# Kernel optimization log

Measured on AMD Instinct MI355X. Metric: run time of the kernel, lower is better.

## Reference

```python
import jax, jax.numpy as jnp
import numpy as np

B, C, D, H, W = 2, 2, 64, 256, 256
EPS = 1e-6
ALPHA = 5.0
TTEMP = 0.7


def _grids():
    gy, gx = jnp.meshgrid(jnp.arange(H, dtype=jnp.float32),
                          jnp.arange(W, dtype=jnp.float32), indexing='ij')
    return gy, gx


def _extract_targets(centerlines, gy, gx):
    # centerlines: [B,1,D,H,W] int labels {0,1,2}. For each (b,d) slice: if label i
    # occurs exactly once, target = (y,x) of that pixel, else negpair (-1,-1).
    cl = centerlines[:, 0]  # [B,D,H,W]
    out = []
    for lbl in (1, 2):
        m = (cl == lbl).astype(jnp.float32)
        cnt = m.sum(axis=(-2, -1))            # [B,D]
        ys = (m * gy).sum(axis=(-2, -1))
        xs = (m * gx).sum(axis=(-2, -1))
        t = jnp.where((cnt == 1.0)[..., None], jnp.stack([ys, xs], axis=-1), -1.0)
        out.append(t)                          # [B,D,2] float32
    return out


def _d2(gy, gx, target):
    # torch PairwiseDistance adds eps to the difference: ||x1-x2+eps||_2
    # -> [B,1,D,H,W]
    dy = gy[None, None, None] - target[:, None, :, 0, None, None] + EPS
    dx = gx[None, None, None] - target[:, None, :, 1, None, None] + EPS
    return jnp.sqrt(dy * dy + dx * dx)


def total_loss(logits, centerlines, radiuses):
    probs = jax.nn.sigmoid(logits)             # [B,2,D,H,W]
    gy, gx = _grids()
    targets = _extract_targets(centerlines, gy, gx)
    d2s = [_d2(gy, gx, t) for t in targets]
    # art masks: relu(exp(d2/r1 - 1) - 1) then filled with 1 where >0  ==  (d2 > r1);
    # the in-place fill makes it gradient-free, so treat as constant {0,1} mask.
    arts = [jax.lax.stop_gradient((d2s[k] > radiuses[k, 1]).astype(jnp.float32))
            for k in range(2)]
    arts = [arts[1], arts[0]]                  # swapped, exactly as in the source
    valid = [(t[:, :, 0] != -1.0).astype(jnp.float32) for t in targets]  # [B,D]

    # ---- CenterDistanceLoss ----
    loss_cent = jnp.float32(0.0)
    for k in range(2):
        art = arts[k]                                            # [B,1,D,H,W]
        denom = (probs * art).sum(axis=(1, 3, 4)) + EPS          # [B,D]
        y_cnt = (art * gy * probs).sum(axis=(1, 3, 4)) / denom
        x_cnt = (art * gx * probs).sum(axis=(1, 3, 4)) / denom
        cnt = jnp.stack([y_cnt, x_cnt], axis=-1)                 # [B,D,2]
        diff = cnt - targets[k] + EPS
        l2 = jnp.sqrt((diff * diff).sum(-1)) * valid[k]
        loss_cent = loss_cent + l2.mean()

    # ---- RadiusConstraintLoss ----
    loss_cnst = jnp.float32(0.0)
    for k in range(2):
        r_lu, r_ow = radiuses[k, 0], radiuses[k, 1]
        vm = valid[k][:, None, :, None, None]                    # [B,1,D,1,1]
        d2 = d2s[k]
        art = arts[k]
        lu_dout = jax.nn.relu(1.0 - jnp.exp(1.0 - d2 / r_lu)) / ALPHA * vm * art
        ow_dout = jax.nn.relu(1.0 - jnp.exp(1.0 - d2 / r_ow)) / ALPHA * vm * art
        p_lu, p_ow = probs[:, :1], probs[:, 1:]
        rc_out = ((lu_dout * p_lu).sum(axis=(1, 3, 4)) / (p_lu.sum(axis=(1, 3, 4)) + EPS)
                  + (ow_dout * p_ow).sum(axis=(1, 3, 4)) / (p_ow.sum(axis=(1, 3, 4)) + EPS))
        lu_din = jax.nn.relu(jnp.exp(1.0 - d2 / r_lu) - 1.0) * vm
        ow_din = jax.nn.relu(jnp.exp(1.0 - d2 / r_ow) - 1.0) * vm
        rc_in = ((lu_din * (1.0 - p_lu)).sum(axis=(1, 3, 4)) / (r_lu * r_lu * jnp.pi)
                 + (ow_din * (1.0 - p_ow)).sum(axis=(1, 3, 4)) / (r_ow * r_ow * jnp.pi))
        loss_cnst = loss_cnst + rc_out.mean() + rc_in.mean()

    # ---- ConsistencyLoss ----  (F.softmax default dim=1 for 5-D; BCE clamps log >= -100)
    p_orig = jax.lax.stop_gradient(jax.nn.softmax(logits[:, :, 1:-1] / TTEMP, axis=1))
    p_shift = jax.nn.softmax(logits[:, :, 0:-2] / TTEMP, axis=1)
    log_p = jnp.maximum(jnp.log(p_orig), -100.0)
    log_1mp = jnp.maximum(jnp.log(1.0 - p_orig), -100.0)
    loss_csis = -(p_shift * log_p + (1.0 - p_shift) * log_1mp).mean()

    return 0.02 * loss_cent + 1.0 * loss_cnst + 0.001 * loss_csis


def setup_inputs():
    key = jax.random.key(0)
    k1, k2, k3, k4, k5 = jax.random.split(key, 5)
    logits = jax.random.normal(k1, (B, C, D, H, W), dtype=jnp.float32)
    # place exactly one ICA(=1) and one ECA(=2) marker per (b,d) slice
    ys1 = jax.random.randint(k2, (B * D,), 0, H)
    xs1 = jax.random.randint(k3, (B * D,), 0, W)
    ys2 = jax.random.randint(k4, (B * D,), 0, H)
    xs2 = jax.random.randint(k5, (B * D,), 0, W)
    bi = jnp.repeat(jnp.arange(B), D)
    di = jnp.tile(jnp.arange(D), B)
    cl = jnp.zeros((B, 1, D, H, W), dtype=jnp.int32)
    cl = cl.at[bi, 0, di, ys1, xs1].set(1)
    cl = cl.at[bi, 0, di, ys2, xs2].set(2)
    cl = cl.at[:, :, 0].set(0)  # exercise the negpair (-1,-1) path
    radiuses = jnp.array([[4.0, 7.0], [5.0, 8.0]], dtype=jnp.float32)
    return {"logits": logits, "centerlines": cl, "radiuses": radiuses}


def reference(logits, centerlines, radiuses):
    return total_loss(logits, centerlines, radiuses)
```

## Files before the change

### kernel.cpp

```cpp
#include <hip/hip_runtime.h>
#include <math.h>

#define BB 2
#define CC 2
#define DD 64
#define HW 65536
#define NROW 128
#define EPSF 1e-6f
#define ALPHAF 5.0f
#define LOG2E 1.44269504089f
#define LN2 0.69314718056f
#define INV_T (1.0f/0.7f)
#define C_SH (INV_T*LOG2E)

struct Ws {
  float tgt[2][NROW][2];
  float valid[2][NROW];
  float part[NROW][2][17];
};

struct RowCtx {
  float t0y, t0x, t1y, t1x;
  float r01sq, r11sq;
  float c00, c01, c10, c11;
};

template<bool N0, bool N1>
__device__ __forceinline__ void do_row(const float4& v0, const float4& v1,
                                       const float4& w0, const float4& w1,
                                       float yf, float x0f,
                                       const RowCtx& cx, float* acc)
{
  const float a0[4] = {v0.x, v0.y, v0.z, v0.w};
  const float a1[4] = {v1.x, v1.y, v1.z, v1.w};
  const float b0[4] = {w0.x, w0.y, w0.z, w0.w};
  const float b1[4] = {w1.x, w1.y, w1.z, w1.w};
  float rp0 = 0.f, rp1 = 0.f, rprod = 0.f, rsp = 0.f, rpsx = 0.f;
  float rA0 = 0.f, rA0x = 0.f, rT00 = 0.f, rT01 = 0.f;
  float rA1 = 0.f, rA1x = 0.f, rT10 = 0.f, rT11 = 0.f;
  const float dy0 = yf - cx.t0y;
  const float dy0sq = dy0 * dy0;
  const float dy1 = yf - cx.t1y;
  const float dy1sq = dy1 * dy1;
#pragma unroll
  for (int e = 0; e < 4; ++e) {
    const float le0 = a0[e], le1 = a1[e];
    const float p0 = __builtin_amdgcn_rcpf(1.f + __expf(-le0));
    const float p1 = __builtin_amdgcn_rcpf(1.f + __expf(-le1));
    rp0 += p0; rp1 += p1;
    const float psum = p0 + p1;
    const float gxf = x0f + (float)e;

    const float t = (le1 - le0) * C_SH;
    const float E = exp2f(-fabsf(t));
    const float R = __builtin_amdgcn_rcpf(1.f + E);
    const float L = log2f(1.f + E);
    const float psig = (t >= 0.f ? E : 1.f) * R;
    const float dorn = (b0[e] - b1[e]) * C_SH;
    rprod = fmaf(psig, dorn, rprod);
    rsp  += fmaxf(-t, 0.f) + L;

    float ap0 = p0, ap1 = p1, bp0 = p0, bp1 = p1;
    float d0sq = 0.f, d1sq = 0.f;
    if (N1) {
      const float dx1 = gxf - cx.t1x;
      d1sq = fmaf(dx1, dx1, dy1sq);
      const float art0 = (d1sq > cx.r11sq) ? 1.f : 0.f;
      ap0 = art0 * p0; ap1 = art0 * p1;
      const float a0p = ap0 + ap1;
      rA0 += a0p; rA0x = fmaf(gxf, a0p, rA0x);
      if (!N0) { rT00 += ap0; rT01 += ap1; }
    }
    if (N0) {
      const float dx0 = gxf - cx.t0x;
      d0sq = fmaf(dx0, dx0, dy0sq);
      const float art1 = (d0sq > cx.r01sq) ? 1.f : 0.f;
      bp0 = art1 * p0; bp1 = art1 * p1;
      const float a1p = bp0 + bp1;
      rA1 += a1p; rA1x = fmaf(gxf, a1p, rA1x);
      if (!N1) { rT10 += bp0; rT11 += bp1; }
    }
    if (!N0 || !N1) rpsx = fmaf(gxf, psum, rpsx);

    if (N0) {
      const float dist0 = __builtin_amdgcn_sqrtf(d0sq);
      const float elu0 = exp2f(fmaf(dist0, -cx.c00, LOG2E));
      const float eow0 = exp2f(fmaf(dist0, -cx.c01, LOG2E));
      acc[8]  = fmaf(fmaxf(1.f - elu0, 0.f), ap0, acc[8]);
      acc[9]  = fmaf(fmaxf(1.f - eow0, 0.f), ap1, acc[9]);
      acc[10] = fmaf(fmaxf(elu0 - 1.f, 0.f), 1.f - p0, acc[10]);
      acc[11] = fmaf(fmaxf(eow0 - 1.f, 0.f), 1.f - p1, acc[11]);
    }
    if (N1) {
      const float dist1 = __builtin_amdgcn_sqrtf(d1sq);
      const float elu1 = exp2f(fmaf(dist1, -cx.c10, LOG2E));
      const float eow1 = exp2f(fmaf(dist1, -cx.c11, LOG2E));
      acc[12] = fmaf(fmaxf(1.f - elu1, 0.f), bp0, acc[12]);
      acc[13] = fmaf(fmaxf(1.f - eow1, 0.f), bp1, acc[13]);
      acc[14] = fmaf(fmaxf(elu1 - 1.f, 0.f), 1.f - p0, acc[14]);
      acc[15] = fmaf(fmaxf(eow1 - 1.f, 0.f), 1.f - p1, acc[15]);
    }
  }
  acc[6] += rp0; acc[7] += rp1; acc[16] += rprod; acc[17] += rsp;
  const float rps = rp0 + rp1;
  if (N1) { acc[0] += rA0; acc[1] = fmaf(yf, rA0, acc[1]); acc[2] += rA0x; }
  else    { acc[0] += rps; acc[1] = fmaf(yf, rps, acc[1]); acc[2] += rpsx; }
  if (N0) { acc[3] += rA1; acc[4] = fmaf(yf, rA1, acc[4]); acc[5] += rA1x; }
  else    { acc[3] += rps; acc[4] = fmaf(yf, rps, acc[4]); acc[5] += rpsx; }
  if (!N0) { acc[8]  += N1 ? rT00 : rp0; acc[9]  += N1 ? rT01 : rp1; }
  if (!N1) { acc[12] += N0 ? rT10 : rp0; acc[13] += N0 ? rT11 : rp1; }
}

#define DISPATCH_ROW(V0,V1,W0,W1,YF)                                       \
  { const bool nr0 = fabsf((YF) - cx.t0y) <= cut0;                         \
    const bool nr1 = fabsf((YF) - cx.t1y) <= cut1;                         \
    if (nr0) { if (nr1) do_row<true ,true >(V0,V1,W0,W1,YF,x0f,cx,acc);    \
               else     do_row<true ,false>(V0,V1,W0,W1,YF,x0f,cx,acc); }  \
    else     { if (nr1) do_row<false,true >(V0,V1,W0,W1,YF,x0f,cx,acc);    \
               else     do_row<false,false>(V0,V1,W0,W1,YF,x0f,cx,acc); } }

__global__ __launch_bounds__(1024) void k_all(const float* __restrict__ logits,
                                              const int* __restrict__ cl,
                                              const float* __restrict__ rad,
                                              Ws* __restrict__ ws)
{
  const int xcd  = blockIdx.x & 7;
  const int slot = blockIdx.x >> 3;
  const int row  = xcd * 16 + (slot >> 1);
  const int half = slot & 1;
  const int tid  = threadIdx.x;
  const int lane = tid & 63;
  const int wid  = tid >> 6;
  const int b = row >> 6, d = row & 63;

  const float* l0 = logits + (((long long)(b * CC + 0) * DD + d) << 16);
  const float* l1 = logits + (((long long)(b * CC + 1) * DD + d) << 16);
  const bool csa = (d < DD - 2);
  const bool csb = (d >= 1) && (d <= DD - 2);
  const long long noff = csa ? HW : 0;
  const float* m0 = l0 + noff;
  const float* m1 = l1 + noff;

  const float x0f = (float)(lane << 2);
  int y = half + (wid << 1);
  int p = (y << 8) + (lane << 2);

  float4 v0 = *(const float4*)(l0 + p);
  float4 v1 = *(const float4*)(l1 + p);
  float4 w0 = *(const float4*)(m0 + p);
  float4 w1 = *(const float4*)(m1 + p);

  __shared__ int sacc[6];
  if (tid < 6) sacc[tid] = 0;
  __syncthreads();
  {
    const int4* cp = (const int4*)(cl + ((long long)row << 16));
#pragma unroll 8
    for (int j = 0; j < 16; ++j) {
      const int idx4 = tid + (j << 10);
      const int4 v = cp[idx4];
      if ((v.x | v.y | v.z | v.w) != 0) {
        const int vv[4] = {v.x, v.y, v.z, v.w};
#pragma unroll
        for (int e = 0; e < 4; ++e) {
          const int val = vv[e];
          if (val == 1 || val == 2) {
            const int hw = (idx4 << 2) + e;
            const int k3 = (val - 1) * 3;
            atomicAdd(&sacc[k3 + 0], 1);
            atomicAdd(&sacc[k3 + 1], hw >> 8);
            atomicAdd(&sacc[k3 + 2], hw & 255);
          }
        }
      }
    }
  }
  __syncthreads();
  const int c0 = sacc[0], c1 = sacc[3];
  const float t0y = (c0 == 1) ? (float)sacc[1] : -1.f;
  const float t0x = (c0 == 1) ? (float)sacc[2] : -1.f;
  const float t1y = (c1 == 1) ? (float)sacc[4] : -1.f;
  const float t1x = (c1 == 1) ? (float)sacc[5] : -1.f;
  if (half == 0 && tid == 0) {
    ws->tgt[0][row][0] = t0y; ws->tgt[0][row][1] = t0x;
    ws->valid[0][row] = (c0 == 1) ? 1.f : 0.f;
    ws->tgt[1][row][0] = t1y; ws->tgt[1][row][1] = t1x;
    ws->valid[1][row] = (c1 == 1) ? 1.f : 0.f;
  }

  const float r00 = rad[0], r01 = rad[1], r10 = rad[2], r11 = rad[3];
  RowCtx cx;
  cx.t0y = t0y - EPSF; cx.t0x = t0x - EPSF;
  cx.t1y = t1y - EPSF; cx.t1x = t1x - EPSF;
  cx.r01sq = r01 * r01; cx.r11sq = r11 * r11;
  cx.c00 = LOG2E / r00; cx.c01 = LOG2E / r01;
  cx.c10 = LOG2E / r10; cx.c11 = LOG2E / r11;
  const float cut0 = 6.f * r01, cut1 = 6.f * r11;

  float acc[18];
#pragma unroll
  for (int i = 0; i < 18; ++i) acc[i] = 0.f;

#pragma unroll 1
  for (int j = 0; j < 7; ++j) {
    const int pn = p + 32 * 256;
    float4 nv0 = *(const float4*)(l0 + pn);
    float4 nv1 = *(const float4*)(l1 + pn);
    float4 nw0 = *(const float4*)(m0 + pn);
    float4 nw1 = *(const float4*)(m1 + pn);
    const float yf = (float)y;
    DISPATCH_ROW(v0, v1, w0, w1, yf);
    v0 = nv0; v1 = nv1; w0 = nw0; w1 = nw1; p = pn; y += 32;
  }
  { const float yf = (float)y;
    DISPATCH_ROW(v0, v1, w0, w1, yf); }

  __shared__ float pl[16][18];
#pragma unroll
  for (int i = 0; i < 18; ++i) {
    float v = acc[i];
#pragma unroll
    for (int off = 32; off > 0; off >>= 1) v += __shfl_down(v, off, 64);
    if (lane == 0) pl[wid][i] = v;
  }
  __syncthreads();
  if (tid < 17) {
    float s;
    if (tid == 16) {
      float prod = 0.f, sp = 0.f;
#pragma unroll
      for (int w = 0; w < 16; ++w) { prod += pl[w][16]; sp += pl[w][17]; }
      s = (csa ? prod * LN2 : 0.f) - (csb ? sp * LN2 : 0.f);
    } else {
      s = 0.f;
#pragma unroll
      for (int w = 0; w < 16; ++w) s += pl[w][tid];
    }
    ws->part[row][half][tid] = s;
  }
}

__global__ void k_final(const float* __restrict__ rad,
                        const Ws* __restrict__ ws, float* __restrict__ out) {
  __shared__ float red[3][NROW];
  const int r = threadIdx.x;
  const float PI = 3.14159265358979323846f;
  float cent = 0.0f, cnst = 0.0f, csis = 0.0f;
  if (r < NROW) {
    float s[17];
#pragma unroll
    for (int i = 0; i < 17; ++i)
      s[i] = ws->part[r][0][i] + ws->part[r][1][i];

    const float P0 = s[6], P1 = s[7];
#pragma unroll
    for (int k = 0; k < 2; ++k) {
      const float vld = ws->valid[k][r];
      const float denom = s[3 * k + 0] + EPSF;
      const float yc = s[3 * k + 1] / denom;
      const float xc = s[3 * k + 2] / denom;
      const float dy = yc - ws->tgt[k][r][0] + EPSF;
      const float dx = xc - ws->tgt[k][r][1] + EPSF;
      cent += sqrtf(dy * dy + dx * dx) * vld;
      const float r_lu = rad[2 * k], r_ow = rad[2 * k + 1];
      const int o = 8 + 4 * k;
      const float rc_out = (s[o]     / (ALPHAF * (P0 + EPSF)) +
                            s[o + 1] / (ALPHAF * (P1 + EPSF))) * vld;
      const float rc_in  = (s[o + 2] / (r_lu * r_lu * PI) +
                            s[o + 3] / (r_ow * r_ow * PI)) * vld;
      cnst += rc_out + rc_in;
    }
    csis = s[16];
  }
  red[0][r] = cent; red[1][r] = cnst; red[2][r] = csis;
  __syncthreads();
  for (int st = NROW / 2; st > 0; st >>= 1) {
    if (r < st) {
      red[0][r] += red[0][r + st];
      red[1][r] += red[1][r + st];
      red[2][r] += red[2][r + st];
    }
    __syncthreads();
  }
  if (r == 0) {
    const float inv_rows = 1.0f / (float)NROW;
    const float loss_cent = red[0][0] * inv_rows;
    const float loss_cnst = red[1][0] * inv_rows;
    const float loss_csis = -red[2][0] / (float)((long long)BB * (DD - 2) * HW);
    out[0] = 0.02f * loss_cent + loss_cnst + 0.001f * loss_csis;
  }
}

extern "C" void kernel_launch(void* const* d_in, const int* in_sizes, int n_in,
                              void* d_out, int out_size, void* d_ws, size_t ws_size,
                              hipStream_t stream) {
  const float* logits = (const float*)d_in[0];
  const int*   cl     = (const int*)d_in[1];
  const float* rad    = (const float*)d_in[2];
  Ws* ws = (Ws*)d_ws;

  k_all<<<2 * NROW, 1024, 0, stream>>>(logits, cl, rad, ws);
  k_final<<<1, NROW, 0, stream>>>(rad, ws, (float*)d_out);
}
```

Before: 37.93 us.

## Split centerline scan across block pair and exchange partials via global flags

Each (b,d) row was previously scanned in full by both blocks assigned to it. Now each block scans half of the label slice, publishes its partial counts and coordinate sums to workspace, and spin-waits on a flag for its partner's partials before combining them. This halves redundant label-read traffic but adds an inter-block spin barrier, a memset launch, and a deadlock risk if the partner blocks are not co-resident (256 blocks of 1024 threads).

```diff
diff --git a/kernel.cpp b/kernel.cpp
--- a/kernel.cpp
+++ b/kernel.cpp
@@ -14,6 +14,8 @@
 #define C_SH (INV_T*LOG2E)
 
 struct Ws {
+  int   flag[NROW][2];
+  int   scanp[NROW][2][6];
   float tgt[2][NROW][2];
   float valid[2][NROW];
   float part[NROW][2][17];
@@ -151,12 +153,13 @@
   float4 w1 = *(const float4*)(m1 + p);
 
   __shared__ int sacc[6];
+  __shared__ float stgt[4];
   if (tid < 6) sacc[tid] = 0;
   __syncthreads();
   {
-    const int4* cp = (const int4*)(cl + ((long long)row << 16));
+    const int4* cp = (const int4*)(cl + ((long long)row << 16) + (half << 15));
 #pragma unroll 8
-    for (int j = 0; j < 16; ++j) {
+    for (int j = 0; j < 8; ++j) {
       const int idx4 = tid + (j << 10);
       const int4 v = cp[idx4];
       if ((v.x | v.y | v.z | v.w) != 0) {
@@ -165,7 +168,7 @@
         for (int e = 0; e < 4; ++e) {
           const int val = vv[e];
           if (val == 1 || val == 2) {
-            const int hw = (idx4 << 2) + e;
+            const int hw = (half << 15) + (idx4 << 2) + e;
             const int k3 = (val - 1) * 3;
             atomicAdd(&sacc[k3 + 0], 1);
             atomicAdd(&sacc[k3 + 1], hw >> 8);
@@ -176,17 +179,32 @@
     }
   }
   __syncthreads();
-  const int c0 = sacc[0], c1 = sacc[3];
-  const float t0y = (c0 == 1) ? (float)sacc[1] : -1.f;
-  const float t0x = (c0 == 1) ? (float)sacc[2] : -1.f;
-  const float t1y = (c1 == 1) ? (float)sacc[4] : -1.f;
-  const float t1x = (c1 == 1) ? (float)sacc[5] : -1.f;
-  if (half == 0 && tid == 0) {
-    ws->tgt[0][row][0] = t0y; ws->tgt[0][row][1] = t0x;
-    ws->valid[0][row] = (c0 == 1) ? 1.f : 0.f;
-    ws->tgt[1][row][0] = t1y; ws->tgt[1][row][1] = t1x;
-    ws->valid[1][row] = (c1 == 1) ? 1.f : 0.f;
-  }
+
+  if (tid == 0) {
+    int* dst = ws->scanp[row][half];
+#pragma unroll
+    for (int i = 0; i < 6; ++i) dst[i] = sacc[i];
+    __threadfence();
+    atomicExch(&ws->flag[row][half], 1);
+    while (atomicAdd(&ws->flag[row][half ^ 1], 0) == 0) {}
+    __threadfence();
+    const int* src = ws->scanp[row][half ^ 1];
+    const int c0 = sacc[0] + src[0];
+    const int c1 = sacc[3] + src[3];
+    const float t0y = (c0 == 1) ? (float)(sacc[1] + src[1]) : -1.f;
+    const float t0x = (c0 == 1) ? (float)(sacc[2] + src[2]) : -1.f;
+    const float t1y = (c1 == 1) ? (float)(sacc[4] + src[4]) : -1.f;
+    const float t1x = (c1 == 1) ? (float)(sacc[5] + src[5]) : -1.f;
+    stgt[0] = t0y; stgt[1] = t0x; stgt[2] = t1y; stgt[3] = t1x;
+    if (half == 0) {
+      ws->tgt[0][row][0] = t0y; ws->tgt[0][row][1] = t0x;
+      ws->valid[0][row] = (c0 == 1) ? 1.f : 0.f;
+      ws->tgt[1][row][0] = t1y; ws->tgt[1][row][1] = t1x;
+      ws->valid[1][row] = (c1 == 1) ? 1.f : 0.f;
+    }
+  }
+  __syncthreads();
+  const float t0y = stgt[0], t0x = stgt[1], t1y = stgt[2], t1x = stgt[3];
 
   const float r00 = rad[0], r01 = rad[1], r10 = rad[2], r11 = rad[3];
   RowCtx cx;
@@ -299,6 +317,7 @@
   const float* rad    = (const float*)d_in[2];
   Ws* ws = (Ws*)d_ws;
 
+  hipMemsetAsync(d_ws, 0, sizeof(int) * NROW * 2, stream);
   k_all<<<2 * NROW, 1024, 0, stream>>>(logits, cl, rad, ws);
   k_final<<<1, NROW, 0, stream>>>(rad, ws, (float*)d_out);
 }
```

Measured after the change: 51.69 us. +36.3%, slower.
